# Kernel optimization log

Hardware: AMD Instinct MI355X
Metric: run time of the kernel (lower is better)

## Reference

```python
import jax, jax.numpy as jnp
from jax import lax
import numpy as np

RADIUS = 1
DILATION = 2
NUM_BINS = 16  # DualSimilarityLoss uses num_bins=16
ALPHA = 5.0
BETA = 0.1
NOISE = 1e-4


def _avg_pool2(x):
    b, c, h, w = x.shape
    return x.reshape(b, c, h // 2, 2, w // 2, 2).mean(axis=(3, 5))


def _conv_rep(x, k, pad):
    # replicate-pad then VALID conv, NCHW / OIHW
    xp = jnp.pad(x, ((0, 0), (0, 0), (pad, pad), (pad, pad)), mode='edge')
    return lax.conv_general_dilated(xp, k, (1, 1), 'VALID',
                                    dimension_numbers=('NCHW', 'OIHW', 'NCHW'))


def _upsample_align_corners(x, H, W):
    # bilinear, align_corners=True (matches F.interpolate(..., align_corners=True))
    b, c, h, w = x.shape

    def coords(n_out, n_in):
        pos = jnp.arange(n_out, dtype=x.dtype) * ((n_in - 1) / (n_out - 1))
        i0 = jnp.clip(jnp.floor(pos).astype(jnp.int32), 0, n_in - 2)
        return i0, pos - i0.astype(x.dtype)

    y0, fy = coords(H, h)
    x0, fx = coords(W, w)
    rows = x[:, :, y0, :] * (1.0 - fy)[None, None, :, None] \
         + x[:, :, y0 + 1, :] * fy[None, None, :, None]
    out = rows[:, :, :, x0] * (1.0 - fx) + rows[:, :, :, x0 + 1] * fx
    return out


def _compute_mind(img, key):
    B, _, H, W = img.shape
    img = _avg_pool2(img)                      # (B,1,H/2,W/2)
    img = img + NOISE * jax.random.normal(key, img.shape, img.dtype)
    h, w = img.shape[2], img.shape[3]
    pad = RADIUS * DILATION                    # 2
    k = 2 * RADIUS + 1                         # 3
    ones_k = jnp.ones((1, 1, k, k), img.dtype)
    padded = jnp.pad(img, ((0, 0), (0, 0), (pad, pad), (pad, pad)), mode='edge')
    patch_mean = lax.conv_general_dilated(padded, ones_k, (1, 1), 'VALID',
                                          dimension_numbers=('NCHW', 'OIHW', 'NCHW')) / (k * k)
    patch_mean = jnp.pad(patch_mean, ((0, 0), (0, 0), (pad, pad), (pad, pad)), mode='edge')
    c = pad
    center = padded[:, :, c:c + h, c:c + w]
    variance = (center - patch_mean[:, :, c:c + h, c:c + w]) ** 2
    variance = _conv_rep(variance, ones_k, RADIUS) / (k * k)
    variance = jnp.maximum(variance, 1e-4)
    descs = []
    for i in range(-RADIUS, RADIUS + 1):
        for j in range(-RADIUS, RADIUS + 1):
            if i == 0 and j == 0:
                continue
            dx, dy = i * DILATION, j * DILATION
            off = padded[:, :, c + dy:c + dy + h, c + dx:c + dx + w]
            diff = jnp.clip((center - off) ** 2 / (variance * 2 + 1e-6), 0.0, 50.0)
            descs.append(diff)
    m = jnp.exp(-jnp.concatenate(descs, axis=1))          # (B,8,h,w)
    m = m / (m.sum(axis=1, keepdims=True) + 1e-8)
    m = jnp.where(jnp.isnan(m), 0.0, m)
    if (h, w) != (H, W):
        m = _upsample_align_corners(m, H, W)
    return m


def _nmi_loss(x, y, kx, ky):
    B = x.shape[0]
    x = x[:, :, ::2, ::2]
    y = y[:, :, ::2, ::2]
    x = x + NOISE * jax.random.normal(kx, x.shape, x.dtype)
    y = y + NOISE * jax.random.normal(ky, y.shape, y.dtype)
    xf = jnp.clip((x.reshape(B, -1) + 1.0) / 2.0, 0.001, 0.999)
    yf = jnp.clip((y.reshape(B, -1) + 1.0) / 2.0, 0.001, 0.999)
    grid = jnp.linspace(0.0, 1.0, NUM_BINS + 1)
    xb = jnp.clip(jnp.searchsorted(grid, xf, side='left') - 1, 0, NUM_BINS - 1)
    yb = jnp.clip(jnp.searchsorted(grid, yf, side='left') - 1, 0, NUM_BINS - 1)
    idx = xb * NUM_BINS + yb                               # (B,N)
    hist = jnp.zeros((B, NUM_BINS * NUM_BINS), jnp.float32)
    hist = hist.at[jnp.arange(B)[:, None], idx].add(1.0)
    hist = hist.reshape(B, NUM_BINS, NUM_BINS)
    hist = hist / (hist.sum(axis=(1, 2), keepdims=True) + 1e-10)
    xh = hist.sum(axis=2)
    yh = hist.sum(axis=1)
    eps = 1e-5
    hist = hist + eps
    xh = xh + eps
    yh = yh + eps
    mi = jnp.sum(hist * (jnp.log(hist) - jnp.log(xh[:, :, None] * yh[:, None, :])), axis=(1, 2))
    hx = -jnp.sum(xh * jnp.log(xh), axis=1)
    hy = -jnp.sum(yh * jnp.log(yh), axis=1)
    se = hx + hy
    nmi = jnp.where(se < 1e-10, 0.0, 2.0 * mi / se)
    nmi = jnp.clip(nmi, -1.0, 1.0)
    return -jnp.clip(nmi.mean(), -1.0, 1.0)


def _reg_loss(flow, ku, kv):
    sx = jnp.array([[-1, 0, 1], [-2, 0, 2], [-1, 0, 1]], jnp.float32).reshape(1, 1, 3, 3)
    sy = jnp.array([[-1, -2, -1], [0, 0, 0], [1, 2, 1]], jnp.float32).reshape(1, 1, 3, 3)
    lp = jnp.array([[0, 1, 0], [1, -4, 1], [0, 1, 0]], jnp.float32).reshape(1, 1, 3, 3)
    f = _avg_pool2(flow)
    u = f[:, 0:1] + NOISE * jax.random.normal(ku, f[:, 0:1].shape, f.dtype)
    v = f[:, 1:2] + NOISE * jax.random.normal(kv, f[:, 1:2].shape, f.dtype)
    grad_mag = _conv_rep(u, sx, 1) ** 2 + _conv_rep(u, sy, 1) ** 2 \
             + _conv_rep(v, sx, 1) ** 2 + _conv_rep(v, sy, 1) ** 2
    lap_mag = _conv_rep(u, lp, 1) ** 2 + _conv_rep(v, lp, 1) ** 2
    return jnp.clip(grad_mag, 0.0, 100.0).mean() + jnp.clip(lap_mag, 0.0, 100.0).mean()


def _total_loss(fixed, moved, flow):
    fixed = jnp.where(jnp.isnan(fixed), 0.0, fixed)
    moved = jnp.where(jnp.isnan(moved), 0.0, moved)
    flow = jnp.where(jnp.isnan(flow), 0.0, flow)
    ks = jax.random.split(jax.random.key(42), 6)
    mi = _nmi_loss(fixed, moved, ks[0], ks[1])
    mx = _compute_mind(fixed, ks[2])
    my = _compute_mind(moved, ks[3])
    d = jnp.abs(mx - my)
    mind = jnp.where(jnp.isnan(d), 0.0, d).mean()
    reg = _reg_loss(flow, ks[4], ks[5])
    return mi + ALPHA * mind + BETA * reg


def setup_inputs() -> dict:
    key = jax.random.key(0)
    k1, k2, k3 = jax.random.split(key, 3)
    B, H, W = 8, 512, 512
    return {
        'fixed': jax.random.normal(k1, (B, 1, H, W), jnp.float32),
        'moved': jax.random.normal(k2, (B, 1, H, W), jnp.float32),
        'flow': jax.random.normal(k3, (B, 2, H, W), jnp.float32),
    }


def reference(fixed, moved, flow):
    return _total_loss(fixed, moved, flow)
```

## Files before the change

### kernel.cpp

```cpp
#include <hip/hip_runtime.h>
#include <cmath>

#define BATCH 8
#define HF 512
#define WF 512
#define HS 256
#define WS 256
#define PLANE_S (HS * WS)
#define PLANE_F (HF * WF)

#define NMIND_BLOCKS 2048
#define NREG_BLOCKS  512

#define OFF_HIST  0
#define OFF_PMIND 8192
#define OFF_PGRAD (OFF_PMIND + NMIND_BLOCKS * 8)
#define OFF_PLAP  (OFF_PGRAD + NREG_BLOCKS * 8)

#define IMG_R 23
#define IMG_S 25
#define T_R 20
#define T_S 21
#define V_R 18
#define V_S 19
#define VP  (V_R * V_S)

#define RP 34
#define RS 35

__device__ __forceinline__ int clampi(int v, int lo, int hi) {
    return v < lo ? lo : (v > hi ? hi : v);
}

__device__ __forceinline__ int bin_of(float x) {
    float v = (x + 1.0f) * 0.5f;
    v = fminf(fmaxf(v, 0.001f), 0.999f);
    float t = v * 16.0f;
    float ft = floorf(t);
    int c = (int)ft + ((t > ft) ? 1 : 0);
    int b = c - 1;
    return b < 0 ? 0 : (b > 15 ? 15 : b);
}

__global__ void init_kernel(unsigned* __restrict__ hist) {
    int t = threadIdx.x;
    for (int i = t; i < BATCH * 256; i += 256) hist[i] = 0u;
}

__global__ __launch_bounds__(256, 6) void fused_main_kernel(
    const float* __restrict__ fixed, const float* __restrict__ moved,
    const float* __restrict__ flow,
    unsigned* __restrict__ hist, double* __restrict__ pmind,
    double* __restrict__ pgrad, double* __restrict__ plap)
{
    __shared__ float S[4570];
    __shared__ unsigned lh[256];
    __shared__ float red[256];
    int tid = threadIdx.x;

    if (blockIdx.x >= NMIND_BLOCKS) {
        int rb = blockIdx.x - NMIND_BLOCKS;
        int b = rb >> 6, rem = rb & 63;
        int tyr = rem >> 3, txr = rem & 7;
        int y0p = tyr * 32, x0p = txr * 32;
        float* U = S;
        float* V = S + RP * RS;
        const float* ur = flow + (size_t)(b * 2) * PLANE_F;
        const float* vr = ur + PLANE_F;
        for (int i = tid; i < RP * RP; i += 256) {
            int r = i / RP, c = i - r * RP;
            int gy = clampi(y0p - 1 + r, 0, HS - 1);
            int gx = clampi(x0p - 1 + c, 0, WS - 1);
            const float* uu = ur + (size_t)(gy * 2) * WF + (size_t)(gx * 2);
            const float* vv = vr + (size_t)(gy * 2) * WF + (size_t)(gx * 2);
            float2 u0 = *(const float2*)uu, u1 = *(const float2*)(uu + WF);
            float2 v0 = *(const float2*)vv, v1 = *(const float2*)(vv + WF);
            U[r * RS + c] = (u0.x + u0.y + u1.x + u1.y) * 0.25f;
            V[r * RS + c] = (v0.x + v0.y + v1.x + v1.y) * 0.25f;
        }
        __syncthreads();
        float g = 0.f, l = 0.f;
        for (int k = tid; k < 32 * 32; k += 256) {
            int y = k >> 5, x = k & 31;
            const float* u0 = &U[y * RS + x];
            const float* v0 = &V[y * RS + x];
            float a00 = u0[0],      a01 = u0[1],          a02 = u0[2];
            float a10 = u0[RS],     a11 = u0[RS + 1],     a12 = u0[RS + 2];
            float a20 = u0[2 * RS], a21 = u0[2 * RS + 1], a22 = u0[2 * RS + 2];
            float c00 = v0[0],      c01 = v0[1],          c02 = v0[2];
            float c10 = v0[RS],     c11 = v0[RS + 1],     c12 = v0[RS + 2];
            float c20 = v0[2 * RS], c21 = v0[2 * RS + 1], c22 = v0[2 * RS + 2];
            float gxu = (a02 - a00) + 2.f * (a12 - a10) + (a22 - a20);
            float gyu = (a20 - a00) + 2.f * (a21 - a01) + (a22 - a02);
            float gxv = (c02 - c00) + 2.f * (c12 - c10) + (c22 - c20);
            float gyv = (c20 - c00) + 2.f * (c21 - c01) + (c22 - c02);
            float lpu = a01 + a10 - 4.f * a11 + a12 + a21;
            float lpv = c01 + c10 - 4.f * c11 + c12 + c21;
            float grad = gxu * gxu + gyu * gyu + gxv * gxv + gyv * gyv;
            float lap = lpu * lpu + lpv * lpv;
            g += fminf(grad, 100.f);
            l += fminf(lap, 100.f);
        }
        red[tid] = g;
        __syncthreads();
        for (int s = 128; s > 0; s >>= 1) { if (tid < s) red[tid] += red[tid + s]; __syncthreads(); }
        if (tid == 0) pgrad[rb] = (double)red[0];
        __syncthreads();
        red[tid] = l;
        __syncthreads();
        for (int s = 128; s > 0; s >>= 1) { if (tid < s) red[tid] += red[tid + s]; __syncthreads(); }
        if (tid == 0) plap[rb] = (double)red[0];
        return;
    }

    int mb = blockIdx.x;
    int b = mb >> 8, rem = mb & 255;
    int ty = rem >> 4, tx = rem & 15;
    const float FS = (float)(255.0 / 511.0);
    int Xb = tx * 32, Yb = ty * 32;
    int dbx = (int)((float)Xb * FS);
    int dby = (int)((float)Yb * FS);
    int ibx = dbx - 3, iby = dby - 3;

    float* imgF = S;
    float* imgM = S + 575;
    float* varF = S + 1150;
    float* varM = S + 1492;
    float* diff = S + 1834;
    float* tF   = diff;
    float* tM   = diff + T_R * T_S;

    lh[tid] = 0u;
    __syncthreads();

    const float* fb = fixed + (size_t)b * PLANE_F;
    const float* mbp = moved + (size_t)b * PLANE_F;
    int oy0 = ty * 16, ox0 = tx * 16;
    for (int i = tid; i < IMG_R * IMG_R; i += 256) {
        int r = i / IMG_R, c = i - r * IMG_R;
        int gy = iby + r, gx = ibx + c;
        int cy = clampi(gy, 0, HS - 1), cx = clampi(gx, 0, WS - 1);
        const float* fp = fb + (size_t)(cy * 2) * WF + (size_t)(cx * 2);
        const float* mp = mbp + (size_t)(cy * 2) * WF + (size_t)(cx * 2);
        float2 f0 = *(const float2*)fp;
        float2 f1 = *(const float2*)(fp + WF);
        float2 m0 = *(const float2*)mp;
        float2 m1 = *(const float2*)(mp + WF);
        imgF[r * IMG_S + c] = (f0.x + f0.y + f1.x + f1.y) * 0.25f;
        imgM[r * IMG_S + c] = (m0.x + m0.y + m1.x + m1.y) * 0.25f;
        if ((unsigned)(gy - oy0) < 16u && (unsigned)(gx - ox0) < 16u) {
            atomicAdd(&lh[bin_of(f0.x) * 16 + bin_of(m0.x)], 1u);
        }
    }
    __syncthreads();
    {
        unsigned v = lh[tid];
        if (v) atomicAdd(&hist[b * 256 + tid], v);
    }

    for (int i = tid; i < T_R * T_R; i += 256) {
        int r = i / T_R, c = i - r * T_R;
        float sF = 0.f, sM = 0.f;
        #pragma unroll
        for (int dy = 0; dy < 3; dy++)
            #pragma unroll
            for (int dx = 0; dx < 3; dx++) {
                sF += imgF[(r + dy) * IMG_S + c + dx];
                sM += imgM[(r + dy) * IMG_S + c + dx];
            }
        float dF = imgF[(r + 2) * IMG_S + c + 2] - sF / 9.0f;
        float dM = imgM[(r + 2) * IMG_S + c + 2] - sM / 9.0f;
        tF[r * T_S + c] = dF * dF;
        tM[r * T_S + c] = dM * dM;
    }
    __syncthreads();

    float vFl[2], vMl[2];
    int vi[2];
    #pragma unroll
    for (int p = 0; p < 2; p++) {
        int i = tid + p * 256;
        vi[p] = -1;
        if (i < V_R * V_R) {
            int r = i / V_R, c = i - r * V_R;
            float sF = 0.f, sM = 0.f;
            #pragma unroll
            for (int dy = 0; dy < 3; dy++)
                #pragma unroll
                for (int dx = 0; dx < 3; dx++) {
                    sF += tF[(r + dy) * T_S + c + dx];
                    sM += tM[(r + dy) * T_S + c + dx];
                }
            vFl[p] = fmaxf(sF / 9.0f, 1e-4f);
            vMl[p] = fmaxf(sM / 9.0f, 1e-4f);
            vi[p] = r * V_S + c;
        }
    }
    __syncthreads();
    #pragma unroll
    for (int p = 0; p < 2; p++) if (vi[p] >= 0) { varF[vi[p]] = vFl[p]; varM[vi[p]] = vMl[p]; }
    __syncthreads();

    for (int i = tid; i < V_R * V_R; i += 256) {
        int r = i / V_R, c = i - r * V_R;
        float cF = imgF[(r + 3) * IMG_S + c + 3];
        float cM = imgM[(r + 3) * IMG_S + c + 3];
        float dF2 = 2.f * varF[r * V_S + c] + 1e-6f;
        float dM2 = 2.f * varM[r * V_S + c] + 1e-6f;
        float eF[8], eM[8];
        float sF = 0.f, sM = 0.f;
        int ch = 0;
        #pragma unroll
        for (int ii = -1; ii <= 1; ii++) {
            #pragma unroll
            for (int jj = -1; jj <= 1; jj++) {
                if (ii == 0 && jj == 0) continue;
                float aF = cF - imgF[(r + 3 + 2 * jj) * IMG_S + (c + 3 + 2 * ii)];
                float aM = cM - imgM[(r + 3 + 2 * jj) * IMG_S + (c + 3 + 2 * ii)];
                float qF = fminf(aF * aF / dF2, 50.f);
                float qM = fminf(aM * aM / dM2, 50.f);
                float vF_ = expf(-qF), vM_ = expf(-qM);
                eF[ch] = vF_; eM[ch] = vM_;
                sF += vF_; sM += vM_;
                ch++;
            }
        }
        float wF = 1.f / (sF + 1e-8f);
        float wM = 1.f / (sM + 1e-8f);
        int base = r * V_S + c;
        #pragma unroll
        for (int q = 0; q < 8; q++) diff[q * VP + base] = eF[q] * wF - eM[q] * wM;
    }
    __syncthreads();

    float local = 0.f;
    for (int k = tid; k < 32 * 32; k += 256) {
        int dy = k >> 5, dx = k & 31;
        float py = (float)(Yb + dy) * FS;
        int y0 = (int)py; if (y0 > HS - 2) y0 = HS - 2;
        float fy = py - (float)y0;
        float px = (float)(Xb + dx) * FS;
        int x0 = (int)px; if (x0 > WS - 2) x0 = WS - 2;
        float fx = px - (float)x0;
        int base = (y0 - dby) * V_S + (x0 - dbx);
        #pragma unroll
        for (int q = 0; q < 8; q++) {
            const float* pq = diff + q * VP + base;
            float a  = pq[0] * (1.f - fy) + pq[V_S] * fy;
            float c2 = pq[1] * (1.f - fy) + pq[V_S + 1] * fy;
            local += fabsf(a * (1.f - fx) + c2 * fx);
        }
    }
    red[tid] = local;
    __syncthreads();
    for (int s = 128; s > 0; s >>= 1) { if (tid < s) red[tid] += red[tid + s]; __syncthreads(); }
    if (tid == 0) pmind[mb] = (double)red[0];
}

__global__ void nmi_final_kernel(const unsigned* __restrict__ hist,
                                 const double* __restrict__ pmind,
                                 const double* __restrict__ pgrad,
                                 const double* __restrict__ plap,
                                 float* __restrict__ out) {
    int t = threadIdx.x;
    __shared__ float p[256];
    __shared__ float xh[16], yh[16];
    __shared__ float red[256];
    __shared__ double redd[256];
    __shared__ float nmi_acc_s;
    if (t == 0) nmi_acc_s = 0.f;
    __syncthreads();

    for (int b = 0; b < BATCH; b++) {
        float pv = (float)hist[b * 256 + t] / 65536.0f;
        p[t] = pv;
        __syncthreads();
        if (t < 16) {
            float s = 0.f;
            for (int j = 0; j < 16; j++) s += p[t * 16 + j];
            xh[t] = s;
        } else if (t < 32) {
            int j = t - 16;
            float s = 0.f;
            for (int i = 0; i < 16; i++) s += p[i * 16 + j];
            yh[j] = s;
        }
        __syncthreads();
        const float eps = 1e-5f;
        int i = t >> 4, j = t & 15;
        float h = pv + eps;
        float mi_term = h * (logf(h) - logf((xh[i] + eps) * (yh[j] + eps)));
        red[t] = mi_term;
        __syncthreads();
        for (int s = 128; s > 0; s >>= 1) { if (t < s) red[t] += red[t + s]; __syncthreads(); }
        float mi = red[0];
        __syncthreads();
        float e_term = 0.f;
        if (t < 16) { float xe = xh[t] + eps; e_term = -xe * logf(xe); }
        else if (t < 32) { float ye = yh[t - 16] + eps; e_term = -ye * logf(ye); }
        red[t] = e_term;
        __syncthreads();
        for (int s = 128; s > 0; s >>= 1) { if (t < s) red[t] += red[t + s]; __syncthreads(); }
        if (t == 0) {
            float se = red[0];
            float nmi = (se < 1e-10f) ? 0.f : 2.f * mi / se;
            nmi_acc_s += fminf(fmaxf(nmi, -1.f), 1.f);
        }
        __syncthreads();
    }

    double sm = 0.0;
    for (int i = t; i < NMIND_BLOCKS; i += 256) sm += pmind[i];
    double sg = 0.0, sl = 0.0;
    for (int i = t; i < NREG_BLOCKS; i += 256) { sg += pgrad[i]; sl += plap[i]; }
    redd[t] = sm;
    __syncthreads();
    for (int s = 128; s > 0; s >>= 1) { if (t < s) redd[t] += redd[t + s]; __syncthreads(); }
    double mind_sum = redd[0];
    __syncthreads();
    redd[t] = sg;
    __syncthreads();
    for (int s = 128; s > 0; s >>= 1) { if (t < s) redd[t] += redd[t + s]; __syncthreads(); }
    double grad_sum = redd[0];
    __syncthreads();
    redd[t] = sl;
    __syncthreads();
    for (int s = 128; s > 0; s >>= 1) { if (t < s) redd[t] += redd[t + s]; __syncthreads(); }
    double lap_sum = redd[0];
    if (t == 0) {
        float s = nmi_acc_s / (float)BATCH;
        s = fminf(fmaxf(s, -1.f), 1.f);
        double mi_loss = -(double)s;
        double mind_mean = mind_sum / (64.0 * (double)PLANE_F);
        double reg = grad_sum / (double)(BATCH * PLANE_S) + lap_sum / (double)(BATCH * PLANE_S);
        out[0] = (float)(mi_loss + 5.0 * mind_mean + 0.1 * reg);
    }
}

extern "C" void kernel_launch(void* const* d_in, const int* in_sizes, int n_in,
                              void* d_out, int out_size, void* d_ws, size_t ws_size,
                              hipStream_t stream) {
    const float* fixed = (const float*)d_in[0];
    const float* moved = (const float*)d_in[1];
    const float* flow  = (const float*)d_in[2];
    float* out = (float*)d_out;
    char* ws = (char*)d_ws;

    unsigned* hist  = (unsigned*)(ws + OFF_HIST);
    double*   pmind = (double*)(ws + OFF_PMIND);
    double*   pgrad = (double*)(ws + OFF_PGRAD);
    double*   plap  = (double*)(ws + OFF_PLAP);

    init_kernel<<<1, 256, 0, stream>>>(hist);
    fused_main_kernel<<<NMIND_BLOCKS + NREG_BLOCKS, 256, 0, stream>>>(
        fixed, moved, flow, hist, pmind, pgrad, plap);
    nmi_final_kernel<<<1, 256, 0, stream>>>(hist, pmind, pgrad, plap, out);
}
```

Before: 120.4 us.

## Fuse final reduction into main kernel via last-block atomic counter

Replaces the separate init and final-reduction kernels with a hipMemsetAsync and a last-block-done pattern: each block increments an atomic counter, and the final block computes NMI and the global sums. It also switches expf to __expf and packs MIND channel differences as float2 for vectorised shared-memory reads during upsampling. This cuts one kernel launch and a serialising tail kernel, at the cost of extra fences and atomics per block and slightly lower exp precision.

```diff
diff --git a/kernel.cpp b/kernel.cpp
--- a/kernel.cpp
+++ b/kernel.cpp
@@ -11,9 +11,11 @@
 
 #define NMIND_BLOCKS 2048
 #define NREG_BLOCKS  512
+#define TOTAL_BLOCKS (NMIND_BLOCKS + NREG_BLOCKS)
 
 #define OFF_HIST  0
-#define OFF_PMIND 8192
+#define OFF_DONE  8192
+#define OFF_PMIND 8256
 #define OFF_PGRAD (OFF_PMIND + NMIND_BLOCKS * 8)
 #define OFF_PLAP  (OFF_PGRAD + NREG_BLOCKS * 8)
 
@@ -42,23 +44,175 @@
     return b < 0 ? 0 : (b > 15 ? 15 : b);
 }
 
-__global__ void init_kernel(unsigned* __restrict__ hist) {
-    int t = threadIdx.x;
-    for (int i = t; i < BATCH * 256; i += 256) hist[i] = 0u;
-}
-
-__global__ __launch_bounds__(256, 6) void fused_main_kernel(
+__global__ __launch_bounds__(256, 6) void fused_all_kernel(
     const float* __restrict__ fixed, const float* __restrict__ moved,
     const float* __restrict__ flow,
-    unsigned* __restrict__ hist, double* __restrict__ pmind,
-    double* __restrict__ pgrad, double* __restrict__ plap)
+    unsigned* __restrict__ hist, unsigned* __restrict__ done,
+    double* __restrict__ pmind, double* __restrict__ pgrad, double* __restrict__ plap,
+    float* __restrict__ out)
 {
     __shared__ float S[4570];
     __shared__ unsigned lh[256];
     __shared__ float red[256];
+    __shared__ unsigned last_flag;
+    __shared__ float nmi_acc_s;
     int tid = threadIdx.x;
 
-    if (blockIdx.x >= NMIND_BLOCKS) {
+    if (blockIdx.x < NMIND_BLOCKS) {
+        int mb = blockIdx.x;
+        int b = mb >> 8, rem = mb & 255;
+        int ty = rem >> 4, tx = rem & 15;
+        const float FS = (float)(255.0 / 511.0);
+        int Xb = tx * 32, Yb = ty * 32;
+        int dbx = (int)((float)Xb * FS);
+        int dby = (int)((float)Yb * FS);
+        int ibx = dbx - 3, iby = dby - 3;
+
+        float* imgF = S;
+        float* imgM = S + 575;
+        float* varF = S + 1150;
+        float* varM = S + 1492;
+        float2* diff2 = (float2*)(S + 1834);
+        float* tF   = S + 1834;
+        float* tM   = tF + T_R * T_S;
+
+        lh[tid] = 0u;
+        __syncthreads();
+
+        const float* fb = fixed + (size_t)b * PLANE_F;
+        const float* mbp = moved + (size_t)b * PLANE_F;
+        int oy0 = ty * 16, ox0 = tx * 16;
+        for (int i = tid; i < IMG_R * IMG_R; i += 256) {
+            int r = i / IMG_R, c = i - r * IMG_R;
+            int gy = iby + r, gx = ibx + c;
+            int cy = clampi(gy, 0, HS - 1), cx = clampi(gx, 0, WS - 1);
+            const float* fp = fb + (size_t)(cy * 2) * WF + (size_t)(cx * 2);
+            const float* mp = mbp + (size_t)(cy * 2) * WF + (size_t)(cx * 2);
+            float2 f0 = *(const float2*)fp;
+            float2 f1 = *(const float2*)(fp + WF);
+            float2 m0 = *(const float2*)mp;
+            float2 m1 = *(const float2*)(mp + WF);
+            imgF[r * IMG_S + c] = (f0.x + f0.y + f1.x + f1.y) * 0.25f;
+            imgM[r * IMG_S + c] = (m0.x + m0.y + m1.x + m1.y) * 0.25f;
+            if ((unsigned)(gy - oy0) < 16u && (unsigned)(gx - ox0) < 16u) {
+                atomicAdd(&lh[bin_of(f0.x) * 16 + bin_of(m0.x)], 1u);
+            }
+        }
+        __syncthreads();
+        {
+            unsigned v = lh[tid];
+            if (v) atomicAdd(&hist[b * 256 + tid], v);
+        }
+
+        for (int i = tid; i < T_R * T_R; i += 256) {
+            int r = i / T_R, c = i - r * T_R;
+            float sF = 0.f, sM = 0.f;
+            #pragma unroll
+            for (int dy = 0; dy < 3; dy++)
+                #pragma unroll
+                for (int dx = 0; dx < 3; dx++) {
+                    sF += imgF[(r + dy) * IMG_S + c + dx];
+                    sM += imgM[(r + dy) * IMG_S + c + dx];
+                }
+            float dF = imgF[(r + 2) * IMG_S + c + 2] - sF / 9.0f;
+            float dM = imgM[(r + 2) * IMG_S + c + 2] - sM / 9.0f;
+            tF[r * T_S + c] = dF * dF;
+            tM[r * T_S + c] = dM * dM;
+        }
+        __syncthreads();
+
+        float vFl[2], vMl[2];
+        int vi[2];
+        #pragma unroll
+        for (int p = 0; p < 2; p++) {
+            int i = tid + p * 256;
+            vi[p] = -1;
+            if (i < V_R * V_R) {
+                int r = i / V_R, c = i - r * V_R;
+                float sF = 0.f, sM = 0.f;
+                #pragma unroll
+                for (int dy = 0; dy < 3; dy++)
+                    #pragma unroll
+                    for (int dx = 0; dx < 3; dx++) {
+                        sF += tF[(r + dy) * T_S + c + dx];
+                        sM += tM[(r + dy) * T_S + c + dx];
+                    }
+                vFl[p] = fmaxf(sF / 9.0f, 1e-4f);
+                vMl[p] = fmaxf(sM / 9.0f, 1e-4f);
+                vi[p] = r * V_S + c;
+            }
+        }
+        __syncthreads();
+        #pragma unroll
+        for (int p = 0; p < 2; p++) if (vi[p] >= 0) { varF[vi[p]] = vFl[p]; varM[vi[p]] = vMl[p]; }
+        __syncthreads();
+
+        for (int i = tid; i < V_R * V_R; i += 256) {
+            int r = i / V_R, c = i - r * V_R;
+            float cF = imgF[(r + 3) * IMG_S + c + 3];
+            float cM = imgM[(r + 3) * IMG_S + c + 3];
+            float dF2 = 2.f * varF[r * V_S + c] + 1e-6f;
+            float dM2 = 2.f * varM[r * V_S + c] + 1e-6f;
+            float eF[8], eM[8];
+            float sF = 0.f, sM = 0.f;
+            int ch = 0;
+            #pragma unroll
+            for (int ii = -1; ii <= 1; ii++) {
+                #pragma unroll
+                for (int jj = -1; jj <= 1; jj++) {
+                    if (ii == 0 && jj == 0) continue;
+                    float aF = cF - imgF[(r + 3 + 2 * jj) * IMG_S + (c + 3 + 2 * ii)];
+                    float aM = cM - imgM[(r + 3 + 2 * jj) * IMG_S + (c + 3 + 2 * ii)];
+                    float qF = fminf(aF * aF / dF2, 50.f);
+                    float qM = fminf(aM * aM / dM2, 50.f);
+                    float vF_ = __expf(-qF), vM_ = __expf(-qM);
+                    eF[ch] = vF_; eM[ch] = vM_;
+                    sF += vF_; sM += vM_;
+                    ch++;
+                }
+            }
+            float wF = 1.f / (sF + 1e-8f);
+            float wM = 1.f / (sM + 1e-8f);
+            int base = r * V_S + c;
+            #pragma unroll
+            for (int q2 = 0; q2 < 4; q2++) {
+                float2 d;
+                d.x = eF[2 * q2]     * wF - eM[2 * q2]     * wM;
+                d.y = eF[2 * q2 + 1] * wF - eM[2 * q2 + 1] * wM;
+                diff2[q2 * VP + base] = d;
+            }
+        }
+        __syncthreads();
+
+        float local = 0.f;
+        for (int k = tid; k < 32 * 32; k += 256) {
+            int dy = k >> 5, dx = k & 31;
+            float py = (float)(Yb + dy) * FS;
+            int y0 = (int)py; if (y0 > HS - 2) y0 = HS - 2;
+            float fy = py - (float)y0;
+            float px = (float)(Xb + dx) * FS;
+            int x0 = (int)px; if (x0 > WS - 2) x0 = WS - 2;
+            float fx = px - (float)x0;
+            float omfy = 1.f - fy, omfx = 1.f - fx;
+            int base = (y0 - dby) * V_S + (x0 - dbx);
+            #pragma unroll
+            for (int q2 = 0; q2 < 4; q2++) {
+                const float2* pq = diff2 + q2 * VP + base;
+                float2 p00 = pq[0], p01 = pq[1];
+                float2 p10 = pq[V_S], p11 = pq[V_S + 1];
+                float ax = p00.x * omfy + p10.x * fy;
+                float bx = p01.x * omfy + p11.x * fy;
+                local += fabsf(ax * omfx + bx * fx);
+                float ay = p00.y * omfy + p10.y * fy;
+                float by = p01.y * omfy + p11.y * fy;
+                local += fabsf(ay * omfx + by * fx);
+            }
+        }
+        red[tid] = local;
+        __syncthreads();
+        for (int s = 128; s > 0; s >>= 1) { if (tid < s) red[tid] += red[tid + s]; __syncthreads(); }
+        if (tid == 0) pmind[mb] = (double)red[0];
+    } else {
         int rb = blockIdx.x - NMIND_BLOCKS;
         int b = rb >> 6, rem = rb & 63;
         int tyr = rem >> 3, txr = rem & 7;
@@ -110,169 +264,28 @@
         __syncthreads();
         for (int s = 128; s > 0; s >>= 1) { if (tid < s) red[tid] += red[tid + s]; __syncthreads(); }
         if (tid == 0) plap[rb] = (double)red[0];
-        return;
-    }
-
-    int mb = blockIdx.x;
-    int b = mb >> 8, rem = mb & 255;
-    int ty = rem >> 4, tx = rem & 15;
-    const float FS = (float)(255.0 / 511.0);
-    int Xb = tx * 32, Yb = ty * 32;
-    int dbx = (int)((float)Xb * FS);
-    int dby = (int)((float)Yb * FS);
-    int ibx = dbx - 3, iby = dby - 3;
-
-    float* imgF = S;
-    float* imgM = S + 575;
-    float* varF = S + 1150;
-    float* varM = S + 1492;
-    float* diff = S + 1834;
-    float* tF   = diff;
-    float* tM   = diff + T_R * T_S;
-
-    lh[tid] = 0u;
-    __syncthreads();
-
-    const float* fb = fixed + (size_t)b * PLANE_F;
-    const float* mbp = moved + (size_t)b * PLANE_F;
-    int oy0 = ty * 16, ox0 = tx * 16;
-    for (int i = tid; i < IMG_R * IMG_R; i += 256) {
-        int r = i / IMG_R, c = i - r * IMG_R;
-        int gy = iby + r, gx = ibx + c;
-        int cy = clampi(gy, 0, HS - 1), cx = clampi(gx, 0, WS - 1);
-        const float* fp = fb + (size_t)(cy * 2) * WF + (size_t)(cx * 2);
-        const float* mp = mbp + (size_t)(cy * 2) * WF + (size_t)(cx * 2);
-        float2 f0 = *(const float2*)fp;
-        float2 f1 = *(const float2*)(fp + WF);
-        float2 m0 = *(const float2*)mp;
-        float2 m1 = *(const float2*)(mp + WF);
-        imgF[r * IMG_S + c] = (f0.x + f0.y + f1.x + f1.y) * 0.25f;
-        imgM[r * IMG_S + c] = (m0.x + m0.y + m1.x + m1.y) * 0.25f;
-        if ((unsigned)(gy - oy0) < 16u && (unsigned)(gx - ox0) < 16u) {
-            atomicAdd(&lh[bin_of(f0.x) * 16 + bin_of(m0.x)], 1u);
-        }
-    }
-    __syncthreads();
-    {
-        unsigned v = lh[tid];
-        if (v) atomicAdd(&hist[b * 256 + tid], v);
-    }
-
-    for (int i = tid; i < T_R * T_R; i += 256) {
-        int r = i / T_R, c = i - r * T_R;
-        float sF = 0.f, sM = 0.f;
-        #pragma unroll
-        for (int dy = 0; dy < 3; dy++)
-            #pragma unroll
-            for (int dx = 0; dx < 3; dx++) {
-                sF += imgF[(r + dy) * IMG_S + c + dx];
-                sM += imgM[(r + dy) * IMG_S + c + dx];
-            }
-        float dF = imgF[(r + 2) * IMG_S + c + 2] - sF / 9.0f;
-        float dM = imgM[(r + 2) * IMG_S + c + 2] - sM / 9.0f;
-        tF[r * T_S + c] = dF * dF;
-        tM[r * T_S + c] = dM * dM;
-    }
-    __syncthreads();
-
-    float vFl[2], vMl[2];
-    int vi[2];
-    #pragma unroll
-    for (int p = 0; p < 2; p++) {
-        int i = tid + p * 256;
-        vi[p] = -1;
-        if (i < V_R * V_R) {
-            int r = i / V_R, c = i - r * V_R;
-            float sF = 0.f, sM = 0.f;
-            #pragma unroll
-            for (int dy = 0; dy < 3; dy++)
-                #pragma unroll
-                for (int dx = 0; dx < 3; dx++) {
-                    sF += tF[(r + dy) * T_S + c + dx];
-                    sM += tM[(r + dy) * T_S + c + dx];
-                }
-            vFl[p] = fmaxf(sF / 9.0f, 1e-4f);
-            vMl[p] = fmaxf(sM / 9.0f, 1e-4f);
-            vi[p] = r * V_S + c;
-        }
-    }
-    __syncthreads();
-    #pragma unroll
-    for (int p = 0; p < 2; p++) if (vi[p] >= 0) { varF[vi[p]] = vFl[p]; varM[vi[p]] = vMl[p]; }
-    __syncthreads();
-
-    for (int i = tid; i < V_R * V_R; i += 256) {
-        int r = i / V_R, c = i - r * V_R;
-        float cF = imgF[(r + 3) * IMG_S + c + 3];
-        float cM = imgM[(r + 3) * IMG_S + c + 3];
-        float dF2 = 2.f * varF[r * V_S + c] + 1e-6f;
-        float dM2 = 2.f * varM[r * V_S + c] + 1e-6f;
-        float eF[8], eM[8];
-        float sF = 0.f, sM = 0.f;
-        int ch = 0;
-        #pragma unroll
-        for (int ii = -1; ii <= 1; ii++) {
-            #pragma unroll
-            for (int jj = -1; jj <= 1; jj++) {
-                if (ii == 0 && jj == 0) continue;
-                float aF = cF - imgF[(r + 3 + 2 * jj) * IMG_S + (c + 3 + 2 * ii)];
-                float aM = cM - imgM[(r + 3 + 2 * jj) * IMG_S + (c + 3 + 2 * ii)];
-                float qF = fminf(aF * aF / dF2, 50.f);
-                float qM = fminf(aM * aM / dM2, 50.f);
-                float vF_ = expf(-qF), vM_ = expf(-qM);
-                eF[ch] = vF_; eM[ch] = vM_;
-                sF += vF_; sM += vM_;
-                ch++;
-            }
-        }
-        float wF = 1.f / (sF + 1e-8f);
-        float wM = 1.f / (sM + 1e-8f);
-        int base = r * V_S + c;
-        #pragma unroll
-        for (int q = 0; q < 8; q++) diff[q * VP + base] = eF[q] * wF - eM[q] * wM;
-    }
-    __syncthreads();
-
-    float local = 0.f;
-    for (int k = tid; k < 32 * 32; k += 256) {
-        int dy = k >> 5, dx = k & 31;
-        float py = (float)(Yb + dy) * FS;
-        int y0 = (int)py; if (y0 > HS - 2) y0 = HS - 2;
-        float fy = py - (float)y0;
-        float px = (float)(Xb + dx) * FS;
-        int x0 = (int)px; if (x0 > WS - 2) x0 = WS - 2;
-        float fx = px - (float)x0;
-        int base = (y0 - dby) * V_S + (x0 - dbx);
-        #pragma unroll
-        for (int q = 0; q < 8; q++) {
-            const float* pq = diff + q * VP + base;
-            float a  = pq[0] * (1.f - fy) + pq[V_S] * fy;
-            float c2 = pq[1] * (1.f - fy) + pq[V_S + 1] * fy;
-            local += fabsf(a * (1.f - fx) + c2 * fx);
-        }
-    }
-    red[tid] = local;
-    __syncthreads();
-    for (int s = 128; s > 0; s >>= 1) { if (tid < s) red[tid] += red[tid + s]; __syncthreads(); }
-    if (tid == 0) pmind[mb] = (double)red[0];
-}
-
-__global__ void nmi_final_kernel(const unsigned* __restrict__ hist,
-                                 const double* __restrict__ pmind,
-                                 const double* __restrict__ pgrad,
-                                 const double* __restrict__ plap,
-                                 float* __restrict__ out) {
-    int t = threadIdx.x;
-    __shared__ float p[256];
-    __shared__ float xh[16], yh[16];
-    __shared__ float red[256];
-    __shared__ double redd[256];
-    __shared__ float nmi_acc_s;
-    if (t == 0) nmi_acc_s = 0.f;
-    __syncthreads();
+    }
+
+    __threadfence();
+    if (tid == 0) {
+        unsigned prev = __hip_atomic_fetch_add(done, 1u, __ATOMIC_ACQ_REL, __HIP_MEMORY_SCOPE_AGENT);
+        last_flag = (prev == TOTAL_BLOCKS - 1) ? 1u : 0u;
+        if (tid == 0 && last_flag) nmi_acc_s = 0.f;
+    }
+    __syncthreads();
+    if (!last_flag) return;
+    __threadfence();
+
+    float* p    = S;
+    float* red2 = S + 256;
+    float* xh   = S + 512;
+    float* yh   = S + 528;
+    double* redd = (double*)(S + 544);
+    int t = tid;
 
     for (int b = 0; b < BATCH; b++) {
-        float pv = (float)hist[b * 256 + t] / 65536.0f;
+        unsigned hv = __hip_atomic_load(&hist[b * 256 + t], __ATOMIC_RELAXED, __HIP_MEMORY_SCOPE_AGENT);
+        float pv = (float)hv / 65536.0f;
         p[t] = pv;
         __syncthreads();
         if (t < 16) {
@@ -290,19 +303,19 @@
         int i = t >> 4, j = t & 15;
         float h = pv + eps;
         float mi_term = h * (logf(h) - logf((xh[i] + eps) * (yh[j] + eps)));
-        red[t] = mi_term;
-        __syncthreads();
-        for (int s = 128; s > 0; s >>= 1) { if (t < s) red[t] += red[t + s]; __syncthreads(); }
-        float mi = red[0];
+        red2[t] = mi_term;
+        __syncthreads();
+        for (int s = 128; s > 0; s >>= 1) { if (t < s) red2[t] += red2[t + s]; __syncthreads(); }
+        float mi = red2[0];
         __syncthreads();
         float e_term = 0.f;
         if (t < 16) { float xe = xh[t] + eps; e_term = -xe * logf(xe); }
         else if (t < 32) { float ye = yh[t - 16] + eps; e_term = -ye * logf(ye); }
-        red[t] = e_term;
-        __syncthreads();
-        for (int s = 128; s > 0; s >>= 1) { if (t < s) red[t] += red[t + s]; __syncthreads(); }
+        red2[t] = e_term;
+        __syncthreads();
+        for (int s = 128; s > 0; s >>= 1) { if (t < s) red2[t] += red2[t + s]; __syncthreads(); }
         if (t == 0) {
-            float se = red[0];
+            float se = red2[0];
             float nmi = (se < 1e-10f) ? 0.f : 2.f * mi / se;
             nmi_acc_s += fminf(fmaxf(nmi, -1.f), 1.f);
         }
@@ -310,9 +323,13 @@
     }
 
     double sm = 0.0;
-    for (int i = t; i < NMIND_BLOCKS; i += 256) sm += pmind[i];
+    for (int i = t; i < NMIND_BLOCKS; i += 256)
+        sm += __hip_atomic_load(&pmind[i], __ATOMIC_RELAXED, __HIP_MEMORY_SCOPE_AGENT);
     double sg = 0.0, sl = 0.0;
-    for (int i = t; i < NREG_BLOCKS; i += 256) { sg += pgrad[i]; sl += plap[i]; }
+    for (int i = t; i < NREG_BLOCKS; i += 256) {
+        sg += __hip_atomic_load(&pgrad[i], __ATOMIC_RELAXED, __HIP_MEMORY_SCOPE_AGENT);
+        sl += __hip_atomic_load(&plap[i],  __ATOMIC_RELAXED, __HIP_MEMORY_SCOPE_AGENT);
+    }
     redd[t] = sm;
     __syncthreads();
     for (int s = 128; s > 0; s >>= 1) { if (t < s) redd[t] += redd[t + s]; __syncthreads(); }
@@ -347,12 +364,13 @@
     char* ws = (char*)d_ws;
 
     unsigned* hist  = (unsigned*)(ws + OFF_HIST);
+    unsigned* done  = (unsigned*)(ws + OFF_DONE);
     double*   pmind = (double*)(ws + OFF_PMIND);
     double*   pgrad = (double*)(ws + OFF_PGRAD);
     double*   plap  = (double*)(ws + OFF_PLAP);
 
-    init_kernel<<<1, 256, 0, stream>>>(hist);
-    fused_main_kernel<<<NMIND_BLOCKS + NREG_BLOCKS, 256, 0, stream>>>(
-        fixed, moved, flow, hist, pmind, pgrad, plap);
-    nmi_final_kernel<<<1, 256, 0, stream>>>(hist, pmind, pgrad, plap, out);
+    hipMemsetAsync(ws + OFF_HIST, 0, OFF_PMIND, stream);
+
+    fused_all_kernel<<<TOTAL_BLOCKS, 256, 0, stream>>>(
+        fixed, moved, flow, hist, done, pmind, pgrad, plap, out);
 }
```

After: 303.2 us. 2.52x slower.

## Replace global histogram atomics with per-block partials and drop init kernel

Applied to the files above, without the earlier changes.

Each MIND block now writes its 256-bin local histogram to a per-block slot, so the global atomics and the separate zeroing kernel are gone. The final single-block kernel sums 256 partials per batch. The diff buffer is stored as float2 pairs so each interpolation does vectorised LDS reads, and expf is swapped for __expf. In exchange the final kernel does serial reduction work over about 2 MB of partials in one block, which may cost more than the launch it removes.

```diff
diff --git a/kernel.cpp b/kernel.cpp
--- a/kernel.cpp
+++ b/kernel.cpp
@@ -11,9 +11,11 @@
 
 #define NMIND_BLOCKS 2048
 #define NREG_BLOCKS  512
-
-#define OFF_HIST  0
-#define OFF_PMIND 8192
+#define TOTAL_BLOCKS (NMIND_BLOCKS + NREG_BLOCKS)
+#define MB (1048576)
+
+#define OFF_HISTP 0
+#define OFF_PMIND (2 * MB)
 #define OFF_PGRAD (OFF_PMIND + NMIND_BLOCKS * 8)
 #define OFF_PLAP  (OFF_PGRAD + NREG_BLOCKS * 8)
 
@@ -42,23 +44,169 @@
     return b < 0 ? 0 : (b > 15 ? 15 : b);
 }
 
-__global__ void init_kernel(unsigned* __restrict__ hist) {
-    int t = threadIdx.x;
-    for (int i = t; i < BATCH * 256; i += 256) hist[i] = 0u;
-}
-
 __global__ __launch_bounds__(256, 6) void fused_main_kernel(
     const float* __restrict__ fixed, const float* __restrict__ moved,
     const float* __restrict__ flow,
-    unsigned* __restrict__ hist, double* __restrict__ pmind,
-    double* __restrict__ pgrad, double* __restrict__ plap)
+    unsigned* __restrict__ hist_part,
+    double* __restrict__ pmind, double* __restrict__ pgrad, double* __restrict__ plap)
 {
     __shared__ float S[4570];
     __shared__ unsigned lh[256];
     __shared__ float red[256];
     int tid = threadIdx.x;
 
-    if (blockIdx.x >= NMIND_BLOCKS) {
+    if (blockIdx.x < NMIND_BLOCKS) {
+        int mb = blockIdx.x;
+        int b = mb >> 8, rem = mb & 255;
+        int ty = rem >> 4, tx = rem & 15;
+        const float FS = (float)(255.0 / 511.0);
+        int Xb = tx * 32, Yb = ty * 32;
+        int dbx = (int)((float)Xb * FS);
+        int dby = (int)((float)Yb * FS);
+        int ibx = dbx - 3, iby = dby - 3;
+
+        float* imgF = S;
+        float* imgM = S + 575;
+        float* varF = S + 1150;
+        float* varM = S + 1492;
+        float2* diff2 = (float2*)(S + 1834);
+        float* tF   = S + 1834;
+        float* tM   = tF + T_R * T_S;
+
+        lh[tid] = 0u;
+        __syncthreads();
+
+        const float* fb = fixed + (size_t)b * PLANE_F;
+        const float* mbp = moved + (size_t)b * PLANE_F;
+        int oy0 = ty * 16, ox0 = tx * 16;
+        for (int i = tid; i < IMG_R * IMG_R; i += 256) {
+            int r = i / IMG_R, c = i - r * IMG_R;
+            int gy = iby + r, gx = ibx + c;
+            int cy = clampi(gy, 0, HS - 1), cx = clampi(gx, 0, WS - 1);
+            const float* fp = fb + (size_t)(cy * 2) * WF + (size_t)(cx * 2);
+            const float* mp = mbp + (size_t)(cy * 2) * WF + (size_t)(cx * 2);
+            float2 f0 = *(const float2*)fp;
+            float2 f1 = *(const float2*)(fp + WF);
+            float2 m0 = *(const float2*)mp;
+            float2 m1 = *(const float2*)(mp + WF);
+            imgF[r * IMG_S + c] = (f0.x + f0.y + f1.x + f1.y) * 0.25f;
+            imgM[r * IMG_S + c] = (m0.x + m0.y + m1.x + m1.y) * 0.25f;
+            if ((unsigned)(gy - oy0) < 16u && (unsigned)(gx - ox0) < 16u) {
+                atomicAdd(&lh[bin_of(f0.x) * 16 + bin_of(m0.x)], 1u);
+            }
+        }
+        __syncthreads();
+        hist_part[(size_t)mb * 256 + tid] = lh[tid];
+
+        for (int i = tid; i < T_R * T_R; i += 256) {
+            int r = i / T_R, c = i - r * T_R;
+            float sF = 0.f, sM = 0.f;
+            #pragma unroll
+            for (int dy = 0; dy < 3; dy++)
+                #pragma unroll
+                for (int dx = 0; dx < 3; dx++) {
+                    sF += imgF[(r + dy) * IMG_S + c + dx];
+                    sM += imgM[(r + dy) * IMG_S + c + dx];
+                }
+            float dF = imgF[(r + 2) * IMG_S + c + 2] - sF / 9.0f;
+            float dM = imgM[(r + 2) * IMG_S + c + 2] - sM / 9.0f;
+            tF[r * T_S + c] = dF * dF;
+            tM[r * T_S + c] = dM * dM;
+        }
+        __syncthreads();
+
+        float vFl[2], vMl[2];
+        int vi[2];
+        #pragma unroll
+        for (int p = 0; p < 2; p++) {
+            int i = tid + p * 256;
+            vi[p] = -1;
+            if (i < V_R * V_R) {
+                int r = i / V_R, c = i - r * V_R;
+                float sF = 0.f, sM = 0.f;
+                #pragma unroll
+                for (int dy = 0; dy < 3; dy++)
+                    #pragma unroll
+                    for (int dx = 0; dx < 3; dx++) {
+                        sF += tF[(r + dy) * T_S + c + dx];
+                        sM += tM[(r + dy) * T_S + c + dx];
+                    }
+                vFl[p] = fmaxf(sF / 9.0f, 1e-4f);
+                vMl[p] = fmaxf(sM / 9.0f, 1e-4f);
+                vi[p] = r * V_S + c;
+            }
+        }
+        __syncthreads();
+        #pragma unroll
+        for (int p = 0; p < 2; p++) if (vi[p] >= 0) { varF[vi[p]] = vFl[p]; varM[vi[p]] = vMl[p]; }
+        __syncthreads();
+
+        for (int i = tid; i < V_R * V_R; i += 256) {
+            int r = i / V_R, c = i - r * V_R;
+            float cF = imgF[(r + 3) * IMG_S + c + 3];
+            float cM = imgM[(r + 3) * IMG_S + c + 3];
+            float dF2 = 2.f * varF[r * V_S + c] + 1e-6f;
+            float dM2 = 2.f * varM[r * V_S + c] + 1e-6f;
+            float eF[8], eM[8];
+            float sF = 0.f, sM = 0.f;
+            int ch = 0;
+            #pragma unroll
+            for (int ii = -1; ii <= 1; ii++) {
+                #pragma unroll
+                for (int jj = -1; jj <= 1; jj++) {
+                    if (ii == 0 && jj == 0) continue;
+                    float aF = cF - imgF[(r + 3 + 2 * jj) * IMG_S + (c + 3 + 2 * ii)];
+                    float aM = cM - imgM[(r + 3 + 2 * jj) * IMG_S + (c + 3 + 2 * ii)];
+                    float qF = fminf(aF * aF / dF2, 50.f);
+                    float qM = fminf(aM * aM / dM2, 50.f);
+                    float vF_ = __expf(-qF), vM_ = __expf(-qM);
+                    eF[ch] = vF_; eM[ch] = vM_;
+                    sF += vF_; sM += vM_;
+                    ch++;
+                }
+            }
+            float wF = 1.f / (sF + 1e-8f);
+            float wM = 1.f / (sM + 1e-8f);
+            int base = r * V_S + c;
+            #pragma unroll
+            for (int q2 = 0; q2 < 4; q2++) {
+                float2 d;
+                d.x = eF[2 * q2]     * wF - eM[2 * q2]     * wM;
+                d.y = eF[2 * q2 + 1] * wF - eM[2 * q2 + 1] * wM;
+                diff2[q2 * VP + base] = d;
+            }
+        }
+        __syncthreads();
+
+        float local = 0.f;
+        for (int k = tid; k < 32 * 32; k += 256) {
+            int dy = k >> 5, dx = k & 31;
+            float py = (float)(Yb + dy) * FS;
+            int y0 = (int)py; if (y0 > HS - 2) y0 = HS - 2;
+            float fy = py - (float)y0;
+            float px = (float)(Xb + dx) * FS;
+            int x0 = (int)px; if (x0 > WS - 2) x0 = WS - 2;
+            float fx = px - (float)x0;
+            float omfy = 1.f - fy, omfx = 1.f - fx;
+            int base = (y0 - dby) * V_S + (x0 - dbx);
+            #pragma unroll
+            for (int q2 = 0; q2 < 4; q2++) {
+                const float2* pq = diff2 + q2 * VP + base;
+                float2 p00 = pq[0], p01 = pq[1];
+                float2 p10 = pq[V_S], p11 = pq[V_S + 1];
+                float ax = p00.x * omfy + p10.x * fy;
+                float bx = p01.x * omfy + p11.x * fy;
+                local += fabsf(ax * omfx + bx * fx);
+                float ay = p00.y * omfy + p10.y * fy;
+                float by = p01.y * omfy + p11.y * fy;
+                local += fabsf(ay * omfx + by * fx);
+            }
+        }
+        red[tid] = local;
+        __syncthreads();
+        for (int s = 128; s > 0; s >>= 1) { if (tid < s) red[tid] += red[tid + s]; __syncthreads(); }
+        if (tid == 0) pmind[mb] = (double)red[0];
+    } else {
         int rb = blockIdx.x - NMIND_BLOCKS;
         int b = rb >> 6, rem = rb & 63;
         int tyr = rem >> 3, txr = rem & 7;
@@ -110,154 +258,10 @@
         __syncthreads();
         for (int s = 128; s > 0; s >>= 1) { if (tid < s) red[tid] += red[tid + s]; __syncthreads(); }
         if (tid == 0) plap[rb] = (double)red[0];
-        return;
     }
-
-    int mb = blockIdx.x;
-    int b = mb >> 8, rem = mb & 255;
-    int ty = rem >> 4, tx = rem & 15;
-    const float FS = (float)(255.0 / 511.0);
-    int Xb = tx * 32, Yb = ty * 32;
-    int dbx = (int)((float)Xb * FS);
-    int dby = (int)((float)Yb * FS);
-    int ibx = dbx - 3, iby = dby - 3;
-
-    float* imgF = S;
-    float* imgM = S + 575;
-    float* varF = S + 1150;
-    float* varM = S + 1492;
-    float* diff = S + 1834;
-    float* tF   = diff;
-    float* tM   = diff + T_R * T_S;
-
-    lh[tid] = 0u;
-    __syncthreads();
-
-    const float* fb = fixed + (size_t)b * PLANE_F;
-    const float* mbp = moved + (size_t)b * PLANE_F;
-    int oy0 = ty * 16, ox0 = tx * 16;
-    for (int i = tid; i < IMG_R * IMG_R; i += 256) {
-        int r = i / IMG_R, c = i - r * IMG_R;
-        int gy = iby + r, gx = ibx + c;
-        int cy = clampi(gy, 0, HS - 1), cx = clampi(gx, 0, WS - 1);
-        const float* fp = fb + (size_t)(cy * 2) * WF + (size_t)(cx * 2);
-        const float* mp = mbp + (size_t)(cy * 2) * WF + (size_t)(cx * 2);
-        float2 f0 = *(const float2*)fp;
-        float2 f1 = *(const float2*)(fp + WF);
-        float2 m0 = *(const float2*)mp;
-        float2 m1 = *(const float2*)(mp + WF);
-        imgF[r * IMG_S + c] = (f0.x + f0.y + f1.x + f1.y) * 0.25f;
-        imgM[r * IMG_S + c] = (m0.x + m0.y + m1.x + m1.y) * 0.25f;
-        if ((unsigned)(gy - oy0) < 16u && (unsigned)(gx - ox0) < 16u) {
-            atomicAdd(&lh[bin_of(f0.x) * 16 + bin_of(m0.x)], 1u);
-        }
-    }
-    __syncthreads();
-    {
-        unsigned v = lh[tid];
-        if (v) atomicAdd(&hist[b * 256 + tid], v);
-    }
-
-    for (int i = tid; i < T_R * T_R; i += 256) {
-        int r = i / T_R, c = i - r * T_R;
-        float sF = 0.f, sM = 0.f;
-        #pragma unroll
-        for (int dy = 0; dy < 3; dy++)
-            #pragma unroll
-            for (int dx = 0; dx < 3; dx++) {
-                sF += imgF[(r + dy) * IMG_S + c + dx];
-                sM += imgM[(r + dy) * IMG_S + c + dx];
-            }
-        float dF = imgF[(r + 2) * IMG_S + c + 2] - sF / 9.0f;
-        float dM = imgM[(r + 2) * IMG_S + c + 2] - sM / 9.0f;
-        tF[r * T_S + c] = dF * dF;
-        tM[r * T_S + c] = dM * dM;
-    }
-    __syncthreads();
-
-    float vFl[2], vMl[2];
-    int vi[2];
-    #pragma unroll
-    for (int p = 0; p < 2; p++) {
-        int i = tid + p * 256;
-        vi[p] = -1;
-        if (i < V_R * V_R) {
-            int r = i / V_R, c = i - r * V_R;
-            float sF = 0.f, sM = 0.f;
-            #pragma unroll
-            for (int dy = 0; dy < 3; dy++)
-                #pragma unroll
-                for (int dx = 0; dx < 3; dx++) {
-                    sF += tF[(r + dy) * T_S + c + dx];
-                    sM += tM[(r + dy) * T_S + c + dx];
-                }
-            vFl[p] = fmaxf(sF / 9.0f, 1e-4f);
-            vMl[p] = fmaxf(sM / 9.0f, 1e-4f);
-            vi[p] = r * V_S + c;
-        }
-    }
-    __syncthreads();
-    #pragma unroll
-    for (int p = 0; p < 2; p++) if (vi[p] >= 0) { varF[vi[p]] = vFl[p]; varM[vi[p]] = vMl[p]; }
-    __syncthreads();
-
-    for (int i = tid; i < V_R * V_R; i += 256) {
-        int r = i / V_R, c = i - r * V_R;
-        float cF = imgF[(r + 3) * IMG_S + c + 3];
-        float cM = imgM[(r + 3) * IMG_S + c + 3];
-        float dF2 = 2.f * varF[r * V_S + c] + 1e-6f;
-        float dM2 = 2.f * varM[r * V_S + c] + 1e-6f;
-        float eF[8], eM[8];
-        float sF = 0.f, sM = 0.f;
-        int ch = 0;
-        #pragma unroll
-        for (int ii = -1; ii <= 1; ii++) {
-            #pragma unroll
-            for (int jj = -1; jj <= 1; jj++) {
-                if (ii == 0 && jj == 0) continue;
-                float aF = cF - imgF[(r + 3 + 2 * jj) * IMG_S + (c + 3 + 2 * ii)];
-                float aM = cM - imgM[(r + 3 + 2 * jj) * IMG_S + (c + 3 + 2 * ii)];
-                float qF = fminf(aF * aF / dF2, 50.f);
-                float qM = fminf(aM * aM / dM2, 50.f);
-                float vF_ = expf(-qF), vM_ = expf(-qM);
-                eF[ch] = vF_; eM[ch] = vM_;
-                sF += vF_; sM += vM_;
-                ch++;
-            }
-        }
-        float wF = 1.f / (sF + 1e-8f);
-        float wM = 1.f / (sM + 1e-8f);
-        int base = r * V_S + c;
-        #pragma unroll
-        for (int q = 0; q < 8; q++) diff[q * VP + base] = eF[q] * wF - eM[q] * wM;
-    }
-    __syncthreads();
-
-    float local = 0.f;
-    for (int k = tid; k < 32 * 32; k += 256) {
-        int dy = k >> 5, dx = k & 31;
-        float py = (float)(Yb + dy) * FS;
-        int y0 = (int)py; if (y0 > HS - 2) y0 = HS - 2;
-        float fy = py - (float)y0;
-        float px = (float)(Xb + dx) * FS;
-        int x0 = (int)px; if (x0 > WS - 2) x0 = WS - 2;
-        float fx = px - (float)x0;
-        int base = (y0 - dby) * V_S + (x0 - dbx);
-        #pragma unroll
-        for (int q = 0; q < 8; q++) {
-            const float* pq = diff + q * VP + base;
-            float a  = pq[0] * (1.f - fy) + pq[V_S] * fy;
-            float c2 = pq[1] * (1.f - fy) + pq[V_S + 1] * fy;
-            local += fabsf(a * (1.f - fx) + c2 * fx);
-        }
-    }
-    red[tid] = local;
-    __syncthreads();
-    for (int s = 128; s > 0; s >>= 1) { if (tid < s) red[tid] += red[tid + s]; __syncthreads(); }
-    if (tid == 0) pmind[mb] = (double)red[0];
-}
-
-__global__ void nmi_final_kernel(const unsigned* __restrict__ hist,
+}
+
+__global__ void nmi_final_kernel(const unsigned* __restrict__ hist_part,
                                  const double* __restrict__ pmind,
                                  const double* __restrict__ pgrad,
                                  const double* __restrict__ plap,
@@ -272,7 +276,10 @@
     __syncthreads();
 
     for (int b = 0; b < BATCH; b++) {
-        float pv = (float)hist[b * 256 + t] / 65536.0f;
+        unsigned hv = 0;
+        const unsigned* hp = hist_part + (size_t)b * 256 * 256 + t;
+        for (int i = 0; i < 256; i++) hv += hp[i * 256];
+        float pv = (float)hv / 65536.0f;
         p[t] = pv;
         __syncthreads();
         if (t < 16) {
@@ -346,13 +353,12 @@
     float* out = (float*)d_out;
     char* ws = (char*)d_ws;
 
-    unsigned* hist  = (unsigned*)(ws + OFF_HIST);
-    double*   pmind = (double*)(ws + OFF_PMIND);
-    double*   pgrad = (double*)(ws + OFF_PGRAD);
-    double*   plap  = (double*)(ws + OFF_PLAP);
-
-    init_kernel<<<1, 256, 0, stream>>>(hist);
-    fused_main_kernel<<<NMIND_BLOCKS + NREG_BLOCKS, 256, 0, stream>>>(
-        fixed, moved, flow, hist, pmind, pgrad, plap);
-    nmi_final_kernel<<<1, 256, 0, stream>>>(hist, pmind, pgrad, plap, out);
-}
+    unsigned* hist_part = (unsigned*)(ws + OFF_HISTP);
+    double*   pmind     = (double*)(ws + OFF_PMIND);
+    double*   pgrad     = (double*)(ws + OFF_PGRAD);
+    double*   plap      = (double*)(ws + OFF_PLAP);
+
+    fused_main_kernel<<<TOTAL_BLOCKS, 256, 0, stream>>>(
+        fixed, moved, flow, hist_part, pmind, pgrad, plap);
+    nmi_final_kernel<<<1, 256, 0, stream>>>(hist_part, pmind, pgrad, plap, out);
+}
```

Result: slower. 180.2 us (+49.7%).
